# Kernel optimization log

Measured on AMD Instinct MI355X. Metric: run time of the kernel, lower is better.

Reference implementation:

```python
import jax, jax.numpy as jnp
import numpy as np

NUM_HEADS = 12
HEAD_DIM = 64
HIDDEN = NUM_HEADS * HEAD_DIM  # 768
B, L = 4, 512

def setup_inputs() -> dict:
    key = jax.random.key(0)
    ks = jax.random.split(key, 8)
    s = 0.02
    return {
        "hidden_states": jax.random.normal(ks[0], (B, L, HIDDEN), jnp.float32),
        "relation_embedding_k": jax.random.normal(ks[1], (B, L, L, HEAD_DIM), jnp.float32),
        "relation_embedding_v": jax.random.normal(ks[2], (B, L, L, HEAD_DIM), jnp.float32),
        "Wq": jax.random.normal(ks[3], (HIDDEN, HIDDEN), jnp.float32) * s,
        "bq": jnp.zeros((HIDDEN,), jnp.float32),
        "Wk": jax.random.normal(ks[4], (HIDDEN, HIDDEN), jnp.float32) * s,
        "bk": jnp.zeros((HIDDEN,), jnp.float32),
        "Wv": jax.random.normal(ks[5], (HIDDEN, HIDDEN), jnp.float32) * s,
        "bv": jnp.zeros((HIDDEN,), jnp.float32),
    }

def _heads(x):
    # [B, L, HIDDEN] -> [B, H, L, D]
    b, l, _ = x.shape
    return x.reshape(b, l, NUM_HEADS, HEAD_DIM).transpose(0, 2, 1, 3)

def reference(hidden_states, relation_embedding_k, relation_embedding_v,
              Wq, bq, Wk, bk, Wv, bv):
    q = _heads(hidden_states @ Wq + bq)  # [B,H,L,D]
    k = _heads(hidden_states @ Wk + bk)
    v = _heads(hidden_states @ Wv + bv)

    # content scores + relation key scores (shared across heads)
    scores = jnp.einsum('bhld,bhmd->bhlm', q, k)
    scores = scores + jnp.einsum('bhld,blrd->bhlr', q, relation_embedding_k)
    scores = scores / np.sqrt(HEAD_DIM).astype(np.float32)

    probs = jax.nn.softmax(scores, axis=-1)  # [B,H,L,L]

    ctx = jnp.einsum('bhlm,bhmd->bhld', probs, v)
    ctx = ctx + jnp.einsum('bhlr,brld->bhld', probs, relation_embedding_v)

    # [B,H,L,D] -> [B,L,HIDDEN]
    b, h, l, d = ctx.shape
    return ctx.transpose(0, 2, 1, 3).reshape(b, l, h * d)
```

## Files before the change

### kernel.cpp

```cpp
#include <hip/hip_runtime.h>
#include <stdint.h>


typedef __attribute__((ext_vector_type(8))) short bf16x8;
typedef __attribute__((ext_vector_type(4))) float f32x4;
typedef __attribute__((ext_vector_type(4))) unsigned int u32x4;

__device__ __forceinline__ unsigned short f2bf(float f) {
  union { float f; unsigned int u; } v; v.f = f;
  unsigned int r = v.u + 0x7fffu + ((v.u >> 16) & 1u);
  return (unsigned short)(r >> 16);
}
__device__ __forceinline__ float bf2f(unsigned short s) {
  union { unsigned int u; float f; } v; v.u = ((unsigned int)s) << 16;
  return v.f;
}
__device__ __forceinline__ void lds_barrier() {
  asm volatile("s_waitcnt lgkmcnt(0)\ns_barrier" ::: "memory");
}
__device__ __forceinline__ unsigned cvtpk(float lo, float hi) {
  unsigned r;
  asm("v_cvt_pk_bf16_f32 %0, %1, %2" : "=v"(r) : "v"(lo), "v"(hi));
  return r;
}

#define GL16(dst, addr, OFF)                                                  \
  asm volatile("global_load_dwordx4 %0, %1, off offset:" #OFF                \
               : "=v"(dst) : "v"(addr))
#define GL4(dst, addr, OFF)                                                   \
  asm volatile("global_load_dword %0, %1, off offset:" #OFF                  \
               : "=v"(dst) : "v"(addr))
#define WAITV(N)                                                              \
  do {                                                                        \
    asm volatile("s_waitcnt vmcnt(" #N ")" ::: "memory");                     \
    __builtin_amdgcn_sched_barrier(0);                                        \
  } while (0)

__global__ void k_cvt_hidden(const float* __restrict__ x, unsigned short* __restrict__ y) {
  int i = blockIdx.x * 256 + threadIdx.x;
  float4 v = reinterpret_cast<const float4*>(x)[i];
  ushort4 o;
  o.x = f2bf(v.x); o.y = f2bf(v.y); o.z = f2bf(v.z); o.w = f2bf(v.w);
  reinterpret_cast<ushort4*>(y)[i] = o;
}

__global__ void k_transp_w(const float* __restrict__ Wq, const float* __restrict__ Wk,
                           const float* __restrict__ Wv, unsigned short* __restrict__ wt) {
  __shared__ float t[64][65];
  const int kt = blockIdx.x, nt = blockIdx.y, wsel = blockIdx.z;
  const float* W = wsel == 0 ? Wq : (wsel == 1 ? Wk : Wv);
  const int lx = threadIdx.x & 63, ly = threadIdx.x >> 6;
  for (int i = 0; i < 64; i += 4)
    t[ly + i][lx] = W[(size_t)(kt * 64 + ly + i) * 768 + nt * 64 + lx];
  __syncthreads();
  for (int i = 0; i < 64; i += 4) {
    int r = ly + i;
    wt[((size_t)wsel * 768 + nt * 64 + r) * 768 + kt * 64 + lx] = f2bf(t[lx][r]);
  }
}

__global__ __launch_bounds__(256) void k_qkv_gemm(
    const unsigned short* __restrict__ A, const unsigned short* __restrict__ Bt,
    const float* __restrict__ bq, const float* __restrict__ bk, const float* __restrict__ bv,
    unsigned short* __restrict__ qbf, unsigned short* __restrict__ kbf,
    unsigned short* __restrict__ vbt) {
  __shared__ __align__(16) unsigned short lA[64 * 64];
  __shared__ __align__(16) unsigned short lB[64 * 64];
  const int tid = threadIdx.x, lane = tid & 63, w = tid >> 6;
  const int m0 = blockIdx.x * 64, n0 = blockIdx.y * 64;
  const int wm = (w >> 1) * 32, wn = (w & 1) * 32;
  f32x4 acc[2][2] = {};

  for (int kt = 0; kt < 12; ++kt) {
    __syncthreads();
#pragma unroll
    for (int i = 0; i < 2; ++i) {
      int e16 = i * 256 + tid;
      int row = e16 >> 3;
      int kb = (e16 & 7) * 16;
      int dst = row * 128 + (kb ^ ((row & 7) << 4));
      u32x4 va = *(const u32x4*)((const char*)A + (size_t)(m0 + row) * 1536 + kt * 128 + kb);
      *(u32x4*)((char*)lA + dst) = va;
      u32x4 vb = *(const u32x4*)((const char*)Bt + (size_t)(n0 + row) * 1536 + kt * 128 + kb);
      *(u32x4*)((char*)lB + dst) = vb;
    }
    __syncthreads();
#pragma unroll
    for (int ks = 0; ks < 2; ++ks) {
      bf16x8 fa[2], fb[2];
      const int kbyte = (ks * 32 + (lane >> 4) * 8) * 2;
#pragma unroll
      for (int mi = 0; mi < 2; ++mi) {
        int row = wm + mi * 16 + (lane & 15);
        fa[mi] = *(const bf16x8*)((const char*)lA + row * 128 + (kbyte ^ ((row & 7) << 4)));
      }
#pragma unroll
      for (int ni = 0; ni < 2; ++ni) {
        int row = wn + ni * 16 + (lane & 15);
        fb[ni] = *(const bf16x8*)((const char*)lB + row * 128 + (kbyte ^ ((row & 7) << 4)));
      }
#pragma unroll
      for (int mi = 0; mi < 2; ++mi)
#pragma unroll
        for (int ni = 0; ni < 2; ++ni)
          acc[mi][ni] = __builtin_amdgcn_mfma_f32_16x16x32_bf16(fa[mi], fb[ni], acc[mi][ni], 0, 0, 0);
    }
  }
#pragma unroll
  for (int mi = 0; mi < 2; ++mi)
#pragma unroll
    for (int ni = 0; ni < 2; ++ni) {
      int gn = n0 + wn + ni * 16 + (lane & 15);
      float bias = (gn < 768) ? bq[gn] : (gn < 1536 ? bk[gn - 768] : bv[gn - 1536]);
#pragma unroll
      for (int r = 0; r < 4; ++r) {
        int gm = m0 + wm + mi * 16 + ((lane >> 4) << 2) + r;
        float val = acc[mi][ni][r] + bias;
        int b = gm >> 9, l = gm & 511;
        int d = gn & 63;
        if (gn < 768) {
          int h = gn >> 6;
          qbf[(((size_t)(b * 12 + h)) * 512 + l) * 64 + d] = f2bf(val);
        } else if (gn < 1536) {
          int h = (gn - 768) >> 6;
          kbf[(((size_t)(b * 12 + h)) * 512 + l) * 64 + d] = f2bf(val);
        } else {
          int h = (gn - 1536) >> 6;
          vbt[(((size_t)(b * 12 + h)) * 64 + d) * 512 + l] = f2bf(val);
        }
      }
    }
}

__global__ __launch_bounds__(256) void k_scores(
    const unsigned short* __restrict__ qbf, const unsigned short* __restrict__ kbf,
    float* __restrict__ S) {
  __shared__ __align__(16) unsigned short lQ[64 * 64];
  __shared__ __align__(16) unsigned short lK[64 * 64];
  const int tid = threadIdx.x, lane = tid & 63, w = tid >> 6;
  const int mt = blockIdx.x, lt = blockIdx.y, bh = blockIdx.z;
  const int wm = (w >> 1) * 32, wn = (w & 1) * 32;
  f32x4 acc[2][2] = {};
#pragma unroll
  for (int i = 0; i < 2; ++i) {
    int e16 = i * 256 + tid;
    int row = e16 >> 3;
    int kb = (e16 & 7) * 16;
    int dst = row * 128 + (kb ^ ((row & 7) << 4));
    u32x4 vq = *(const u32x4*)((const char*)qbf + ((size_t)bh * 512 + lt * 64 + row) * 128 + kb);
    *(u32x4*)((char*)lQ + dst) = vq;
    u32x4 vk = *(const u32x4*)((const char*)kbf + ((size_t)bh * 512 + mt * 64 + row) * 128 + kb);
    *(u32x4*)((char*)lK + dst) = vk;
  }
  __syncthreads();
#pragma unroll
  for (int ks = 0; ks < 2; ++ks) {
    bf16x8 fa[2], fb[2];
    const int kbyte = (ks * 32 + (lane >> 4) * 8) * 2;
#pragma unroll
    for (int mi = 0; mi < 2; ++mi) {
      int row = wm + mi * 16 + (lane & 15);
      fa[mi] = *(const bf16x8*)((const char*)lQ + row * 128 + (kbyte ^ ((row & 7) << 4)));
    }
#pragma unroll
    for (int ni = 0; ni < 2; ++ni) {
      int row = wn + ni * 16 + (lane & 15);
      fb[ni] = *(const bf16x8*)((const char*)lK + row * 128 + (kbyte ^ ((row & 7) << 4)));
    }
#pragma unroll
    for (int mi = 0; mi < 2; ++mi)
#pragma unroll
      for (int ni = 0; ni < 2; ++ni)
        acc[mi][ni] = __builtin_amdgcn_mfma_f32_16x16x32_bf16(fa[mi], fb[ni], acc[mi][ni], 0, 0, 0);
  }
#pragma unroll
  for (int mi = 0; mi < 2; ++mi)
#pragma unroll
    for (int ni = 0; ni < 2; ++ni) {
      int gm = mt * 64 + wn + ni * 16 + (lane & 15);
#pragma unroll
      for (int r = 0; r < 4; ++r) {
        int gl = lt * 64 + wm + mi * 16 + ((lane >> 4) << 2) + r;
        S[(size_t)bh * 262144 + (size_t)gl * 512 + gm] = acc[mi][ni][r];
      }
    }
}

__global__ __launch_bounds__(256) void k_rel(
    const unsigned short* __restrict__ qbf,
    const float* __restrict__ relk,
    const float* __restrict__ relv,
    const float* __restrict__ S,
    unsigned short* __restrict__ pbf,
    float* __restrict__ crel) {
  __shared__ __align__(16) char X[24576];
  const int tid = threadIdx.x, lane = tid & 63, w = tid >> 6;
  const int bl = blockIdx.x, b = bl >> 9, l = bl & 511;
  const int lm = lane & 15, lg = lane >> 4;
  const int hq = lm < 12 ? lm : 11;

  union { f32x4 f; bf16x8 b; } qa0, qa1;
  const char* aQ = (const char*)qbf + (((size_t)b * 12 + hq) * 512 + l) * 128 + (size_t)lg * 16;
  GL16(qa0.f, aQ, 0);
  GL16(qa1.f, aQ, 64);

  float sreg[3][8];
  const char* aS = (const char*)S + ((((size_t)b * 12 + w * 3) * 512 + l) * 512 + lane) * 4;
#define SRLOAD(hh)                                                            \
  do {                                                                        \
    const char* p_ = aS + (size_t)(hh) * 1048576;                             \
    GL4(sreg[hh][0], p_, 0);    GL4(sreg[hh][1], p_, 256);                    \
    GL4(sreg[hh][2], p_, 512);  GL4(sreg[hh][3], p_, 768);                    \
    GL4(sreg[hh][4], p_, 1024); GL4(sreg[hh][5], p_, 1280);                   \
    GL4(sreg[hh][6], p_, 1536); GL4(sreg[hh][7], p_, 1792);                   \
  } while (0)
  SRLOAD(0); SRLOAD(1); SRLOAD(2);

  const char* aA = (const char*)relk + (size_t)bl * 131072 +
                   (size_t)(w * 128 + lm) * 256 + (size_t)lg * 32;
  f32x4 td[3][4];
#define TISSUE(t, s)                                                          \
  do {                                                                        \
    const char* p_ = aA + (size_t)(t) * 4096;                                 \
    GL16(td[s][0], p_, 0);   GL16(td[s][1], p_, 16);                          \
    GL16(td[s][2], p_, 128); GL16(td[s][3], p_, 144);                         \
  } while (0)
  TISSUE(0, 0);
  TISSUE(1, 1);

#define ACONSUME(t, s)                                                        \
  do {                                                                        \
    union { bf16x8 v; unsigned u[4]; } fb0, fb1;                              \
    fb0.u[0] = cvtpk(td[s][0][0], td[s][0][1]);                               \
    fb0.u[1] = cvtpk(td[s][0][2], td[s][0][3]);                               \
    fb0.u[2] = cvtpk(td[s][1][0], td[s][1][1]);                               \
    fb0.u[3] = cvtpk(td[s][1][2], td[s][1][3]);                               \
    fb1.u[0] = cvtpk(td[s][2][0], td[s][2][1]);                               \
    fb1.u[1] = cvtpk(td[s][2][2], td[s][2][3]);                               \
    fb1.u[2] = cvtpk(td[s][3][0], td[s][3][1]);                               \
    fb1.u[3] = cvtpk(td[s][3][2], td[s][3][3]);                               \
    f32x4 acc = {0.f, 0.f, 0.f, 0.f};                                         \
    acc = __builtin_amdgcn_mfma_f32_16x16x32_bf16(qa0.b, fb0.v, acc, 0, 0, 0);\
    acc = __builtin_amdgcn_mfma_f32_16x16x32_bf16(qa1.b, fb1.v, acc, 0, 0, 0);\
    if (lg < 3) {                                                             \
      const int r_ = w * 128 + (t) * 16 + lm;                                 \
      _Pragma("unroll")                                                       \
      for (int reg = 0; reg < 4; ++reg)                                       \
        *(float*)(X + (lg * 4 + reg) * 2048 + ((r_ * 4) ^ (lg << 6))) =       \
            acc[reg];                                                         \
    }                                                                         \
  } while (0)

  TISSUE(2, 2); WAITV(8); ACONSUME(0, 0);
  TISSUE(3, 0); WAITV(8); ACONSUME(1, 1);
  TISSUE(4, 1); WAITV(8); ACONSUME(2, 2);
  TISSUE(5, 2); WAITV(8); ACONSUME(3, 0);
  TISSUE(6, 0); WAITV(8); ACONSUME(4, 1);
  TISSUE(7, 1); WAITV(8); ACONSUME(5, 2);
  WAITV(4); ACONSUME(6, 0);
  WAITV(0); ACONSUME(7, 1);

  lds_barrier();

#pragma unroll
  for (int hh = 0; hh < 3; ++hh) {
    const int h = w * 3 + hh;
    const int sw = ((h >> 2) & 3) << 6;
    float sv[8];
    float mx = -1e30f;
#pragma unroll
    for (int j = 0; j < 8; ++j) {
      const int r = j * 64 + lane;
      float s = (*(const float*)(X + h * 2048 + ((r * 4) ^ sw)) + sreg[hh][j]) * 0.125f;
      sv[j] = s;
      mx = fmaxf(mx, s);
    }
#pragma unroll
    for (int off = 32; off; off >>= 1) mx = fmaxf(mx, __shfl_xor(mx, off));
    float sm = 0.f;
#pragma unroll
    for (int j = 0; j < 8; ++j) { sv[j] = __expf(sv[j] - mx); sm += sv[j]; }
#pragma unroll
    for (int off = 32; off; off >>= 1) sm += __shfl_xor(sm, off);
    const float inv = 1.f / sm;
#pragma unroll
    for (int j = 0; j < 8; ++j) {
      const int r = j * 64 + lane;
      *(float*)(X + h * 2048 + ((r * 4) ^ sw)) = sv[j] * inv;
    }
  }
  lds_barrier();

  const char* aV[8];
#pragma unroll
  for (int j = 0; j < 8; ++j)
    aV[j] = (const char*)relv + (size_t)b * 67108864 +
            (size_t)(w * 128 + j) * 131072 + (size_t)l * 256 + (size_t)lane * 4;
  float vv[3][8];
#define CISSUE(m, s)                                                          \
  do {                                                                        \
    GL4(vv[s][0], aV[0] + (size_t)(m) * 1048576, 0);                          \
    GL4(vv[s][1], aV[1] + (size_t)(m) * 1048576, 0);                          \
    GL4(vv[s][2], aV[2] + (size_t)(m) * 1048576, 0);                          \
    GL4(vv[s][3], aV[3] + (size_t)(m) * 1048576, 0);                          \
    GL4(vv[s][4], aV[4] + (size_t)(m) * 1048576, 0);                          \
    GL4(vv[s][5], aV[5] + (size_t)(m) * 1048576, 0);                          \
    GL4(vv[s][6], aV[6] + (size_t)(m) * 1048576, 0);                          \
    GL4(vv[s][7], aV[7] + (size_t)(m) * 1048576, 0);                          \
  } while (0)

  float cacc[12];
#pragma unroll
  for (int h = 0; h < 12; ++h) cacc[h] = 0.f;

#define CCONSUME(g, s)                                                        \
  do {                                                                        \
    _Pragma("unroll")                                                         \
    for (int q = 0; q < 2; ++q) {                                             \
      const int rb = w * 512 + (g) * 32 + q * 16;                             \
      _Pragma("unroll")                                                       \
      for (int h = 0; h < 12; ++h) {                                          \
        const f32x4 p =                                                       \
            *(const f32x4*)(X + h * 2048 + (rb ^ (((h >> 2) & 3) << 6)));     \
        cacc[h] += p[0] * vv[s][q * 4 + 0] + p[1] * vv[s][q * 4 + 1] +        \
                   p[2] * vv[s][q * 4 + 2] + p[3] * vv[s][q * 4 + 3];         \
      }                                                                       \
    }                                                                         \
  } while (0)

  CISSUE(0, 0);
  CISSUE(1, 1);
  CISSUE(2, 2);  WAITV(16); CCONSUME(0, 0);
  CISSUE(3, 0);  WAITV(16); CCONSUME(1, 1);
  CISSUE(4, 1);  WAITV(16); CCONSUME(2, 2);
  CISSUE(5, 2);  WAITV(16); CCONSUME(3, 0);
  CISSUE(6, 0);  WAITV(16); CCONSUME(4, 1);
  CISSUE(7, 1);  WAITV(16); CCONSUME(5, 2);
  CISSUE(8, 2);  WAITV(16); CCONSUME(6, 0);
  CISSUE(9, 0);  WAITV(16); CCONSUME(7, 1);
  CISSUE(10, 1); WAITV(16); CCONSUME(8, 2);
  CISSUE(11, 2); WAITV(16); CCONSUME(9, 0);
  CISSUE(12, 0); WAITV(16); CCONSUME(10, 1);
  CISSUE(13, 1); WAITV(16); CCONSUME(11, 2);
  CISSUE(14, 2); WAITV(16); CCONSUME(12, 0);
  CISSUE(15, 0); WAITV(16); CCONSUME(13, 1);
  WAITV(8);  CCONSUME(14, 2);
  WAITV(0);  CCONSUME(15, 0);

  lds_barrier();

#pragma unroll
  for (int hh = 0; hh < 3; ++hh) {
    const int h = w * 3 + hh;
    const int sw = ((h >> 2) & 3) << 6;
    const size_t srow = (((size_t)b * 12 + h) * 512 + l) * 512;
#pragma unroll
    for (int j = 0; j < 8; ++j) {
      const int r = j * 64 + lane;
      pbf[srow + r] = f2bf(*(const float*)(X + h * 2048 + ((r * 4) ^ sw)));
    }
  }
  lds_barrier();

  float* red = (float*)X;
#pragma unroll
  for (int h = 0; h < 12; ++h) red[(w * 12 + h) * 64 + lane] = cacc[h];
  lds_barrier();
  for (int i = tid; i < 768; i += 256) {
    const int h = i >> 6, d = i & 63;
    crel[(size_t)bl * 768 + i] =
        red[h * 64 + d] + red[(12 + h) * 64 + d] + red[(24 + h) * 64 + d] + red[(36 + h) * 64 + d];
  }
#undef SRLOAD
#undef TISSUE
#undef ACONSUME
#undef CISSUE
#undef CCONSUME
}

__global__ __launch_bounds__(256) void k_pv(
    const unsigned short* __restrict__ pbf, const unsigned short* __restrict__ vbt,
    const float* __restrict__ crel, float* __restrict__ out) {
  __shared__ __align__(16) unsigned short lP[64 * 64];
  __shared__ __align__(16) unsigned short lV[64 * 64];
  const int tid = threadIdx.x, lane = tid & 63, w = tid >> 6;
  const int lt = blockIdx.x, bh = blockIdx.y;
  const int b = bh / 12, h = bh % 12;
  const int wm = (w >> 1) * 32, wn = (w & 1) * 32;
  f32x4 acc[2][2] = {};
  const char* pbase = (const char*)pbf + ((size_t)bh * 512 + lt * 64) * 1024;
  const char* vbase = (const char*)vbt + (size_t)bh * 64 * 1024;
  for (int kt = 0; kt < 8; ++kt) {
    __syncthreads();
#pragma unroll
    for (int i = 0; i < 2; ++i) {
      int e16 = i * 256 + tid;
      int row = e16 >> 3;
      int kb = (e16 & 7) * 16;
      int dst = row * 128 + (kb ^ ((row & 7) << 4));
      u32x4 vp = *(const u32x4*)(pbase + (size_t)row * 1024 + kt * 128 + kb);
      *(u32x4*)((char*)lP + dst) = vp;
      u32x4 vv = *(const u32x4*)(vbase + (size_t)row * 1024 + kt * 128 + kb);
      *(u32x4*)((char*)lV + dst) = vv;
    }
    __syncthreads();
#pragma unroll
    for (int ks = 0; ks < 2; ++ks) {
      bf16x8 fa[2], fb[2];
      const int kbyte = (ks * 32 + (lane >> 4) * 8) * 2;
#pragma unroll
      for (int mi = 0; mi < 2; ++mi) {
        int row = wm + mi * 16 + (lane & 15);
        fa[mi] = *(const bf16x8*)((const char*)lP + row * 128 + (kbyte ^ ((row & 7) << 4)));
      }
#pragma unroll
      for (int ni = 0; ni < 2; ++ni) {
        int row = wn + ni * 16 + (lane & 15);
        fb[ni] = *(const bf16x8*)((const char*)lV + row * 128 + (kbyte ^ ((row & 7) << 4)));
      }
#pragma unroll
      for (int mi = 0; mi < 2; ++mi)
#pragma unroll
        for (int ni = 0; ni < 2; ++ni)
          acc[mi][ni] = __builtin_amdgcn_mfma_f32_16x16x32_bf16(fa[mi], fb[ni], acc[mi][ni], 0, 0, 0);
    }
  }
#pragma unroll
  for (int mi = 0; mi < 2; ++mi)
#pragma unroll
    for (int ni = 0; ni < 2; ++ni) {
      int gd = wn + ni * 16 + (lane & 15);
#pragma unroll
      for (int r = 0; r < 4; ++r) {
        int gl = lt * 64 + wm + mi * 16 + ((lane >> 4) << 2) + r;
        size_t o = ((size_t)b * 512 + gl) * 768 + h * 64 + gd;
        out[o] = acc[mi][ni][r] + crel[o];
      }
    }
}

extern "C" void kernel_launch(void* const* d_in, const int* in_sizes, int n_in,
                              void* d_out, int out_size, void* d_ws, size_t ws_size,
                              hipStream_t stream) {
  (void)in_sizes; (void)n_in; (void)out_size; (void)ws_size;
  const float* hidden = (const float*)d_in[0];
  const float* relk   = (const float*)d_in[1];
  const float* relv   = (const float*)d_in[2];
  const float* Wq     = (const float*)d_in[3];
  const float* bq     = (const float*)d_in[4];
  const float* Wk     = (const float*)d_in[5];
  const float* bk     = (const float*)d_in[6];
  const float* Wv     = (const float*)d_in[7];
  const float* bv     = (const float*)d_in[8];
  float* out = (float*)d_out;
  char* ws = (char*)d_ws;

  unsigned short* hb  = (unsigned short*)(ws);
  unsigned short* wt  = (unsigned short*)(ws + 3145728);
  unsigned short* qbf = (unsigned short*)(ws + 6684672);
  unsigned short* kbf = (unsigned short*)(ws + 9830400);
  unsigned short* vbt = (unsigned short*)(ws + 12976128);
  float*          S   = (float*)(ws + 16121856);
  unsigned short* pbf = (unsigned short*)(ws + 66453504);
  float*          cr  = (float*)(ws + 91619328);

  k_cvt_hidden<<<1536, 256, 0, stream>>>(hidden, hb);
  k_transp_w<<<dim3(12, 12, 3), 256, 0, stream>>>(Wq, Wk, Wv, wt);
  k_qkv_gemm<<<dim3(32, 36), 256, 0, stream>>>(hb, wt, bq, bk, bv, qbf, kbf, vbt);
  k_scores<<<dim3(8, 8, 48), 256, 0, stream>>>(qbf, kbf, S);
  k_rel<<<2048, 256, 0, stream>>>(qbf, relk, relv, S, pbf, cr);
  k_pv<<<dim3(8, 48), 256, 0, stream>>>(pbf, vbt, cr, out);
}
```

Baseline: 194.6 us.

## Split relation kernel into score-softmax and relv contraction with wider loads

The fused k_rel kernel is split into k_relA (relation-key scores, softmax and bf16 probs, reading S directly instead of prefetching it) and a new k_relv kernel. k_relv tiles 16 query rows by 128 relation rows, stages the bf16 probs in LDS and streams relv with 16-byte loads. It writes four partial context buffers into the reused S workspace, and k_pv sums them. The intent is to replace the strided 4-byte relv loads with wide coalesced ones and to give each stage its own occupancy. The cost is an extra kernel launch, a global round trip of the probabilities, and extra partial-buffer traffic.

New measurement: 196.5 us. No clear change (+1.0%).

```diff
diff --git a/kernel.cpp b/kernel.cpp
--- a/kernel.cpp
+++ b/kernel.cpp
@@ -26,9 +26,6 @@
 
 #define GL16(dst, addr, OFF)                                                  \
   asm volatile("global_load_dwordx4 %0, %1, off offset:" #OFF                \
-               : "=v"(dst) : "v"(addr))
-#define GL4(dst, addr, OFF)                                                   \
-  asm volatile("global_load_dword %0, %1, off offset:" #OFF                  \
                : "=v"(dst) : "v"(addr))
 #define WAITV(N)                                                              \
   do {                                                                        \
@@ -186,13 +183,11 @@
     }
 }
 
-__global__ __launch_bounds__(256) void k_rel(
+__global__ __launch_bounds__(256) void k_relA(
     const unsigned short* __restrict__ qbf,
     const float* __restrict__ relk,
-    const float* __restrict__ relv,
     const float* __restrict__ S,
-    unsigned short* __restrict__ pbf,
-    float* __restrict__ crel) {
+    unsigned short* __restrict__ pbf) {
   __shared__ __align__(16) char X[24576];
   const int tid = threadIdx.x, lane = tid & 63, w = tid >> 6;
   const int bl = blockIdx.x, b = bl >> 9, l = bl & 511;
@@ -204,30 +199,15 @@
   GL16(qa0.f, aQ, 0);
   GL16(qa1.f, aQ, 64);
 
-  float sreg[3][8];
-  const char* aS = (const char*)S + ((((size_t)b * 12 + w * 3) * 512 + l) * 512 + lane) * 4;
-#define SRLOAD(hh)                                                            \
-  do {                                                                        \
-    const char* p_ = aS + (size_t)(hh) * 1048576;                             \
-    GL4(sreg[hh][0], p_, 0);    GL4(sreg[hh][1], p_, 256);                    \
-    GL4(sreg[hh][2], p_, 512);  GL4(sreg[hh][3], p_, 768);                    \
-    GL4(sreg[hh][4], p_, 1024); GL4(sreg[hh][5], p_, 1280);                   \
-    GL4(sreg[hh][6], p_, 1536); GL4(sreg[hh][7], p_, 1792);                   \
-  } while (0)
-  SRLOAD(0); SRLOAD(1); SRLOAD(2);
-
   const char* aA = (const char*)relk + (size_t)bl * 131072 +
                    (size_t)(w * 128 + lm) * 256 + (size_t)lg * 32;
-  f32x4 td[3][4];
+  f32x4 td[2][4];
 #define TISSUE(t, s)                                                          \
   do {                                                                        \
     const char* p_ = aA + (size_t)(t) * 4096;                                 \
     GL16(td[s][0], p_, 0);   GL16(td[s][1], p_, 16);                          \
     GL16(td[s][2], p_, 128); GL16(td[s][3], p_, 144);                         \
   } while (0)
-  TISSUE(0, 0);
-  TISSUE(1, 1);
-
 #define ACONSUME(t, s)                                                        \
   do {                                                                        \
     union { bf16x8 v; unsigned u[4]; } fb0, fb1;                              \
@@ -251,101 +231,17 @@
     }                                                                         \
   } while (0)
 
-  TISSUE(2, 2); WAITV(8); ACONSUME(0, 0);
-  TISSUE(3, 0); WAITV(8); ACONSUME(1, 1);
-  TISSUE(4, 1); WAITV(8); ACONSUME(2, 2);
-  TISSUE(5, 2); WAITV(8); ACONSUME(3, 0);
-  TISSUE(6, 0); WAITV(8); ACONSUME(4, 1);
-  TISSUE(7, 1); WAITV(8); ACONSUME(5, 2);
+  TISSUE(0, 0); TISSUE(1, 1);
+  WAITV(4); ACONSUME(0, 0); TISSUE(2, 0);
+  WAITV(4); ACONSUME(1, 1); TISSUE(3, 1);
+  WAITV(4); ACONSUME(2, 0); TISSUE(4, 0);
+  WAITV(4); ACONSUME(3, 1); TISSUE(5, 1);
+  WAITV(4); ACONSUME(4, 0); TISSUE(6, 0);
+  WAITV(4); ACONSUME(5, 1); TISSUE(7, 1);
   WAITV(4); ACONSUME(6, 0);
   WAITV(0); ACONSUME(7, 1);
-
-  lds_barrier();
-
-#pragma unroll
-  for (int hh = 0; hh < 3; ++hh) {
-    const int h = w * 3 + hh;
-    const int sw = ((h >> 2) & 3) << 6;
-    float sv[8];
-    float mx = -1e30f;
-#pragma unroll
-    for (int j = 0; j < 8; ++j) {
-      const int r = j * 64 + lane;
-      float s = (*(const float*)(X + h * 2048 + ((r * 4) ^ sw)) + sreg[hh][j]) * 0.125f;
-      sv[j] = s;
-      mx = fmaxf(mx, s);
-    }
-#pragma unroll
-    for (int off = 32; off; off >>= 1) mx = fmaxf(mx, __shfl_xor(mx, off));
-    float sm = 0.f;
-#pragma unroll
-    for (int j = 0; j < 8; ++j) { sv[j] = __expf(sv[j] - mx); sm += sv[j]; }
-#pragma unroll
-    for (int off = 32; off; off >>= 1) sm += __shfl_xor(sm, off);
-    const float inv = 1.f / sm;
-#pragma unroll
-    for (int j = 0; j < 8; ++j) {
-      const int r = j * 64 + lane;
-      *(float*)(X + h * 2048 + ((r * 4) ^ sw)) = sv[j] * inv;
-    }
-  }
-  lds_barrier();
-
-  const char* aV[8];
-#pragma unroll
-  for (int j = 0; j < 8; ++j)
-    aV[j] = (const char*)relv + (size_t)b * 67108864 +
-            (size_t)(w * 128 + j) * 131072 + (size_t)l * 256 + (size_t)lane * 4;
-  float vv[3][8];
-#define CISSUE(m, s)                                                          \
-  do {                                                                        \
-    GL4(vv[s][0], aV[0] + (size_t)(m) * 1048576, 0);                          \
-    GL4(vv[s][1], aV[1] + (size_t)(m) * 1048576, 0);                          \
-    GL4(vv[s][2], aV[2] + (size_t)(m) * 1048576, 0);                          \
-    GL4(vv[s][3], aV[3] + (size_t)(m) * 1048576, 0);                          \
-    GL4(vv[s][4], aV[4] + (size_t)(m) * 1048576, 0);                          \
-    GL4(vv[s][5], aV[5] + (size_t)(m) * 1048576, 0);                          \
-    GL4(vv[s][6], aV[6] + (size_t)(m) * 1048576, 0);                          \
-    GL4(vv[s][7], aV[7] + (size_t)(m) * 1048576, 0);                          \
-  } while (0)
-
-  float cacc[12];
-#pragma unroll
-  for (int h = 0; h < 12; ++h) cacc[h] = 0.f;
-
-#define CCONSUME(g, s)                                                        \
-  do {                                                                        \
-    _Pragma("unroll")                                                         \
-    for (int q = 0; q < 2; ++q) {                                             \
-      const int rb = w * 512 + (g) * 32 + q * 16;                             \
-      _Pragma("unroll")                                                       \
-      for (int h = 0; h < 12; ++h) {                                          \
-        const f32x4 p =                                                       \
-            *(const f32x4*)(X + h * 2048 + (rb ^ (((h >> 2) & 3) << 6)));     \
-        cacc[h] += p[0] * vv[s][q * 4 + 0] + p[1] * vv[s][q * 4 + 1] +        \
-                   p[2] * vv[s][q * 4 + 2] + p[3] * vv[s][q * 4 + 3];         \
-      }                                                                       \
-    }                                                                         \
-  } while (0)
-
-  CISSUE(0, 0);
-  CISSUE(1, 1);
-  CISSUE(2, 2);  WAITV(16); CCONSUME(0, 0);
-  CISSUE(3, 0);  WAITV(16); CCONSUME(1, 1);
-  CISSUE(4, 1);  WAITV(16); CCONSUME(2, 2);
-  CISSUE(5, 2);  WAITV(16); CCONSUME(3, 0);
-  CISSUE(6, 0);  WAITV(16); CCONSUME(4, 1);
-  CISSUE(7, 1);  WAITV(16); CCONSUME(5, 2);
-  CISSUE(8, 2);  WAITV(16); CCONSUME(6, 0);
-  CISSUE(9, 0);  WAITV(16); CCONSUME(7, 1);
-  CISSUE(10, 1); WAITV(16); CCONSUME(8, 2);
-  CISSUE(11, 2); WAITV(16); CCONSUME(9, 0);
-  CISSUE(12, 0); WAITV(16); CCONSUME(10, 1);
-  CISSUE(13, 1); WAITV(16); CCONSUME(11, 2);
-  CISSUE(14, 2); WAITV(16); CCONSUME(12, 0);
-  CISSUE(15, 0); WAITV(16); CCONSUME(13, 1);
-  WAITV(8);  CCONSUME(14, 2);
-  WAITV(0);  CCONSUME(15, 0);
+#undef TISSUE
+#undef ACONSUME
 
   lds_barrier();
 
@@ -354,33 +250,118 @@
     const int h = w * 3 + hh;
     const int sw = ((h >> 2) & 3) << 6;
     const size_t srow = (((size_t)b * 12 + h) * 512 + l) * 512;
+    const float* sp = S + srow + lane;
+    float sv[8];
+    float mx = -1e30f;
 #pragma unroll
     for (int j = 0; j < 8; ++j) {
       const int r = j * 64 + lane;
-      pbf[srow + r] = f2bf(*(const float*)(X + h * 2048 + ((r * 4) ^ sw)));
-    }
-  }
-  lds_barrier();
-
-  float* red = (float*)X;
-#pragma unroll
-  for (int h = 0; h < 12; ++h) red[(w * 12 + h) * 64 + lane] = cacc[h];
-  lds_barrier();
-  for (int i = tid; i < 768; i += 256) {
-    const int h = i >> 6, d = i & 63;
-    crel[(size_t)bl * 768 + i] =
-        red[h * 64 + d] + red[(12 + h) * 64 + d] + red[(24 + h) * 64 + d] + red[(36 + h) * 64 + d];
-  }
-#undef SRLOAD
-#undef TISSUE
-#undef ACONSUME
-#undef CISSUE
-#undef CCONSUME
+      float s = (*(const float*)(X + h * 2048 + ((r * 4) ^ sw)) + sp[j * 64]) * 0.125f;
+      sv[j] = s;
+      mx = fmaxf(mx, s);
+    }
+#pragma unroll
+    for (int off = 32; off; off >>= 1) mx = fmaxf(mx, __shfl_xor(mx, off));
+    float sm = 0.f;
+#pragma unroll
+    for (int j = 0; j < 8; ++j) { sv[j] = __expf(sv[j] - mx); sm += sv[j]; }
+#pragma unroll
+    for (int off = 32; off; off >>= 1) sm += __shfl_xor(sm, off);
+    const float inv = 1.f / sm;
+#pragma unroll
+    for (int j = 0; j < 8; ++j)
+      pbf[srow + j * 64 + lane] = f2bf(sv[j] * inv);
+  }
+}
+
+__global__ __launch_bounds__(256) void k_relv(
+    const unsigned short* __restrict__ pbf,
+    const float* __restrict__ relv,
+    float* __restrict__ part) {
+  __shared__ __align__(16) char PS[49152];
+  const int tid = threadIdx.x, lane = tid & 63, w = tid >> 6;
+  const int lg = blockIdx.x, rc = blockIdx.y, b = blockIdx.z;
+  const int l0 = lg * 16, r0 = rc * 128;
+
+  {
+    const int x = tid & 15, rowb = tid >> 4;
+#pragma unroll
+    for (int pass = 0; pass < 12; ++pass) {
+      const int ri = pass * 16 + rowb;
+      const int h = ri >> 4, lr = ri & 15;
+      const char* src = (const char*)pbf +
+          ((((size_t)b * 12 + h) * 512 + l0 + lr) * 512 + r0) * 2 + (size_t)x * 16;
+      u32x4 v = *(const u32x4*)src;
+      *(u32x4*)(PS + h * 4096 + lr * 256 + ((x * 16) ^ ((lr & 3) << 4))) = v;
+    }
+  }
+  __syncthreads();
+
+  const int lr_w = w * 4 + (lane >> 4);
+  const int l = l0 + lr_w;
+  const char* rvb = (const char*)relv +
+      (((size_t)b * 512 + r0) * 512 + l) * 256 + (size_t)(lane & 15) * 16;
+
+  f32x4 vA[8], vB[8];
+  f32x4 acc[12];
+#pragma unroll
+  for (int h = 0; h < 12; ++h) acc[h] = {0.f, 0.f, 0.f, 0.f};
+
+#define VISSUE(o, buf)                                                        \
+  do {                                                                        \
+    GL16(buf[0], rvb + (size_t)((o) * 8 + 0) * 131072, 0);                    \
+    GL16(buf[1], rvb + (size_t)((o) * 8 + 1) * 131072, 0);                    \
+    GL16(buf[2], rvb + (size_t)((o) * 8 + 2) * 131072, 0);                    \
+    GL16(buf[3], rvb + (size_t)((o) * 8 + 3) * 131072, 0);                    \
+    GL16(buf[4], rvb + (size_t)((o) * 8 + 4) * 131072, 0);                    \
+    GL16(buf[5], rvb + (size_t)((o) * 8 + 5) * 131072, 0);                    \
+    GL16(buf[6], rvb + (size_t)((o) * 8 + 6) * 131072, 0);                    \
+    GL16(buf[7], rvb + (size_t)((o) * 8 + 7) * 131072, 0);                    \
+  } while (0)
+#define VCONS(o, buf)                                                         \
+  do {                                                                        \
+    _Pragma("unroll")                                                         \
+    for (int h = 0; h < 12; ++h) {                                            \
+      bf16x8 p8 = *(const bf16x8*)(PS + h * 4096 + lr_w * 256 +               \
+                                   (((o) * 16) ^ ((lr_w & 3) << 4)));         \
+      _Pragma("unroll")                                                       \
+      for (int j = 0; j < 8; ++j) {                                           \
+        const float pf = bf2f((unsigned short)p8[j]);                         \
+        acc[h] += pf * buf[j];                                                \
+      }                                                                       \
+    }                                                                         \
+  } while (0)
+
+  VISSUE(0, vA);
+  VISSUE(1, vB);
+  WAITV(8); VCONS(0, vA); VISSUE(2, vA);
+  WAITV(8); VCONS(1, vB); VISSUE(3, vB);
+  WAITV(8); VCONS(2, vA); VISSUE(4, vA);
+  WAITV(8); VCONS(3, vB); VISSUE(5, vB);
+  WAITV(8); VCONS(4, vA); VISSUE(6, vA);
+  WAITV(8); VCONS(5, vB); VISSUE(7, vB);
+  WAITV(8); VCONS(6, vA); VISSUE(8, vA);
+  WAITV(8); VCONS(7, vB); VISSUE(9, vB);
+  WAITV(8); VCONS(8, vA); VISSUE(10, vA);
+  WAITV(8); VCONS(9, vB); VISSUE(11, vB);
+  WAITV(8); VCONS(10, vA); VISSUE(12, vA);
+  WAITV(8); VCONS(11, vB); VISSUE(13, vB);
+  WAITV(8); VCONS(12, vA); VISSUE(14, vA);
+  WAITV(8); VCONS(13, vB); VISSUE(15, vB);
+  WAITV(8); VCONS(14, vA);
+  WAITV(0); VCONS(15, vB);
+#undef VISSUE
+#undef VCONS
+
+  float* op = part + ((size_t)rc * 2048 + (size_t)b * 512 + l) * 768 + (lane & 15) * 4;
+#pragma unroll
+  for (int h = 0; h < 12; ++h)
+    *(f32x4*)(op + h * 64) = acc[h];
 }
 
 __global__ __launch_bounds__(256) void k_pv(
     const unsigned short* __restrict__ pbf, const unsigned short* __restrict__ vbt,
-    const float* __restrict__ crel, float* __restrict__ out) {
+    const float* __restrict__ part, float* __restrict__ out) {
   __shared__ __align__(16) unsigned short lP[64 * 64];
   __shared__ __align__(16) unsigned short lV[64 * 64];
   const int tid = threadIdx.x, lane = tid & 63, w = tid >> 6;
@@ -434,7 +415,8 @@
       for (int r = 0; r < 4; ++r) {
         int gl = lt * 64 + wm + mi * 16 + ((lane >> 4) << 2) + r;
         size_t o = ((size_t)b * 512 + gl) * 768 + h * 64 + gd;
-        out[o] = acc[mi][ni][r] + crel[o];
+        out[o] = acc[mi][ni][r] + part[o] + part[o + 1572864] +
+                 part[o + 2 * 1572864] + part[o + 3 * 1572864];
       }
     }
 }
@@ -461,13 +443,14 @@
   unsigned short* kbf = (unsigned short*)(ws + 9830400);
   unsigned short* vbt = (unsigned short*)(ws + 12976128);
   float*          S   = (float*)(ws + 16121856);
+  float*          part= (float*)(ws + 16121856);
   unsigned short* pbf = (unsigned short*)(ws + 66453504);
-  float*          cr  = (float*)(ws + 91619328);
 
   k_cvt_hidden<<<1536, 256, 0, stream>>>(hidden, hb);
   k_transp_w<<<dim3(12, 12, 3), 256, 0, stream>>>(Wq, Wk, Wv, wt);
   k_qkv_gemm<<<dim3(32, 36), 256, 0, stream>>>(hb, wt, bq, bk, bv, qbf, kbf, vbt);
   k_scores<<<dim3(8, 8, 48), 256, 0, stream>>>(qbf, kbf, S);
-  k_rel<<<2048, 256, 0, stream>>>(qbf, relk, relv, S, pbf, cr);
-  k_pv<<<dim3(8, 48), 256, 0, stream>>>(pbf, vbt, cr, out);
-}
+  k_relA<<<2048, 256, 0, stream>>>(qbf, relk, S, pbf);
+  k_relv<<<dim3(32, 4, 4), 256, 0, stream>>>(pbf, relv, part);
+  k_pv<<<dim3(8, 48), 256, 0, stream>>>(pbf, vbt, part, out);
+}
```
